# Optimization experiments

Hardware: AMD Instinct MI355X
Metric: run time of the kernel (lower is better)

The kernel has to match this reference:

```python
import jax, jax.numpy as jnp
import numpy as np

EPS = 1e-5  # torch BatchNorm1d default eps
N_NODES, N_EDGES, F_IN, HID, N_LAYERS = 100000, 1600000, 128, 128, 3


def batchnorm(x):
    # affine=False, track_running_stats=False -> normalize with batch stats (biased var)
    m = x.mean(axis=0)
    v = x.var(axis=0)
    return (x - m) / jnp.sqrt(v + EPS)


def gcn_conv(x, W, b, src, dst, deg_inv_sqrt, n):
    # PyG GCNConv: add self-loops, symmetric norm D^-1/2 (A+I) D^-1/2, then linear.
    h = x @ W  # [N, H]
    norm = deg_inv_sqrt[src] * deg_inv_sqrt[dst]  # [E]
    agg = jax.ops.segment_sum(h[src] * norm[:, None], dst, num_segments=n)
    agg = agg + h * (deg_inv_sqrt ** 2)[:, None]  # self-loop term (norm = 1/deg_i)
    return agg + b


def setup_inputs() -> dict:
    key = jax.random.key(0)
    ks = jax.random.split(key, 12)
    x = jax.random.normal(ks[0], (N_NODES, F_IN), dtype=jnp.float32)
    edge_index = jax.random.randint(ks[1], (2, N_EDGES), 0, N_NODES, dtype=jnp.int32)
    s = 1.0 / np.sqrt(F_IN)
    W0 = jax.random.uniform(ks[2], (F_IN, HID), jnp.float32, -s, s)
    b0 = jax.random.uniform(ks[3], (HID,), jnp.float32, -s, s)
    sh = 1.0 / np.sqrt(HID)
    Ws = jax.random.uniform(ks[4], (N_LAYERS - 1, HID, HID), jnp.float32, -sh, sh)
    bs = jax.random.uniform(ks[5], (N_LAYERS - 1, HID), jnp.float32, -sh, sh)
    lin1_w = jax.random.uniform(ks[6], (HID, HID), jnp.float32, -sh, sh)
    lin1_b = jax.random.uniform(ks[7], (HID,), jnp.float32, -sh, sh)
    lin2_w = jax.random.uniform(ks[8], (HID, 2), jnp.float32, -sh, sh)
    lin2_b = jax.random.uniform(ks[9], (2,), jnp.float32, -sh, sh)
    return {"x": x, "edge_index": edge_index, "W0": W0, "b0": b0, "Ws": Ws,
            "bs": bs, "lin1_w": lin1_w, "lin1_b": lin1_b, "lin2_w": lin2_w, "lin2_b": lin2_b}


def reference(x, edge_index, W0, b0, Ws, bs, lin1_w, lin1_b, lin2_w, lin2_b):
    n = x.shape[0]
    src, dst = edge_index[0], edge_index[1]
    # degree with self-loops (computed on target nodes, as in PyG)
    deg = jax.ops.segment_sum(jnp.ones_like(dst, dtype=x.dtype), dst, num_segments=n) + 1.0
    deg_inv_sqrt = deg ** -0.5
    x = jax.nn.relu(batchnorm(gcn_conv(x, W0, b0, src, dst, deg_inv_sqrt, n)))
    for i in range(Ws.shape[0]):
        x = jax.nn.relu(batchnorm(gcn_conv(x, Ws[i], bs[i], src, dst, deg_inv_sqrt, n)))
    x = jax.nn.relu(batchnorm(x @ lin1_w + lin1_b))
    return x @ lin2_w + lin2_b
```

## Files before the change

### kernel.cpp

```cpp
#include <hip/hip_runtime.h>
#include <hip/hip_fp16.h>
#include <math.h>

#define HID 128
#define EPS 1e-5f
#define NBUCK 256
#define BCAP 10240
#define TILE 8192

typedef _Float16 half8 __attribute__((ext_vector_type(8)));
typedef _Float16 half4v __attribute__((ext_vector_type(4)));
typedef float f32x4 __attribute__((ext_vector_type(4)));

__global__ __launch_bounds__(256) void setup(float* __restrict__ psums,
                                             const float* __restrict__ W0,
                                             const float* __restrict__ Ws,
                                             const float* __restrict__ lin1w,
                                             _Float16* __restrict__ Wht,
                                             int* __restrict__ bcur,
                                             _Float16* __restrict__ zrow) {
    int g = blockIdx.x * 256 + threadIdx.x;
    if (g < 4 * 65536) psums[g] = 0.f;
    if (g < 65536) {
        int m = g >> 14;
        int idx = g & 16383;
        int n = idx >> 7, k = idx & 127;
        const float* W = (m == 0) ? W0 : (m == 1) ? Ws : (m == 2) ? (Ws + 16384) : lin1w;
        Wht[(size_t)m * 16384 + n * 128 + k] = (_Float16)W[k * 128 + n];
    }
    if (g < NBUCK) bcur[g] = 0;
    if (g < 128) zrow[g] = (_Float16)0.f;
}

__global__ __launch_bounds__(512) void bin_edges(const int* __restrict__ src, const int* __restrict__ dst,
                                                 int* __restrict__ bcur, int* __restrict__ pairPack, int E) {
    __shared__ int lpack[TILE];
    __shared__ unsigned char lbuck[TILE];
    __shared__ int hist[NBUCK], hscan[NBUCK], cur[NBUCK], delta[NBUCK];
    const int t = threadIdx.x;
    const int base = blockIdx.x * TILE;

    if (t < NBUCK) hist[t] = 0;
    __syncthreads();

    int pk[16], bk[16];
#pragma unroll
    for (int i = 0; i < 16; ++i) {
        int e = base + t + 512 * i;
        if (e < E) {
            int s = src[e], d = dst[e];
            pk[i] = (s << 9) | (d & 511);
            bk[i] = d >> 9;
            atomicAdd(&hist[bk[i]], 1);
        } else {
            bk[i] = -1;
        }
    }
    __syncthreads();

    int v = (t < NBUCK) ? hist[t] : 0;
    if (t < NBUCK) hscan[t] = v;
    __syncthreads();
    for (int off = 1; off < NBUCK; off <<= 1) {
        int u = (t >= off && t < NBUCK) ? hscan[t - off] : 0;
        __syncthreads();
        if (t < NBUCK) hscan[t] += u;
        __syncthreads();
    }
    if (t < NBUCK) cur[t] = hscan[t] - v;
    __syncthreads();

#pragma unroll
    for (int i = 0; i < 16; ++i) {
        if (bk[i] >= 0) {
            int p = atomicAdd(&cur[bk[i]], 1);
            lpack[p] = pk[i];
            lbuck[p] = (unsigned char)bk[i];
        }
    }
    __syncthreads();

    if (t < NBUCK) {
        int c = hist[t];
        if (c > 0) {
            int gbase = t * BCAP + atomicAdd(&bcur[t], c);
            delta[t] = gbase - (hscan[t] - c);
        }
    }
    __syncthreads();

    int total = hscan[NBUCK - 1];
    for (int i = t; i < total; i += 512) {
        int b = lbuck[i];
        pairPack[delta[b] + i] = lpack[i];
    }
}

__global__ __launch_bounds__(512) void bucket_csr(const int* __restrict__ pairPack,
                                                  const int* __restrict__ bcur,
                                                  int* __restrict__ cnt, float* __restrict__ dis,
                                                  int* __restrict__ rowptr,
                                                  int* __restrict__ srcsort, int N) {
    __shared__ int spair[BCAP];
    __shared__ int deg[512], sc[512], cur[512];
    const int b = blockIdx.x;
    const int t = threadIdx.x;
    deg[t] = 0;
    __syncthreads();
    int n = bcur[b];
    if (n > BCAP) n = BCAP;
    const int base = b * BCAP;
    for (int i = t; i < n; i += 512) {
        int p = pairPack[base + i];
        spair[i] = p;
        atomicAdd(&deg[p & 511], 1);
    }
    __syncthreads();
    int node = b * 512 + t;
    int d = deg[t];
    sc[t] = d;
    __syncthreads();
    for (int off = 1; off < 512; off <<= 1) {
        int u = (t >= off) ? sc[t - off] : 0;
        __syncthreads();
        sc[t] += u;
        __syncthreads();
    }
    int myoff = sc[t] - d;
    cur[t] = myoff;
    if (node < N) {
        cnt[node] = d;
        dis[node] = rsqrtf((float)d + 1.0f);
        rowptr[node] = base + myoff;
    }
    __syncthreads();
    for (int i = t; i < n; i += 512) {
        int p = spair[i];
        int pos = atomicAdd(&cur[p & 511], 1);
        srcsort[base + pos] = p >> 9;
    }
}

template <bool INF16, bool NORM, bool SCALEOUT, bool STATS>
__global__ __launch_bounds__(512) void gemm_mfma(const float* __restrict__ Xf,
                                                 const _Float16* __restrict__ Xh,
                                                 const _Float16* __restrict__ Wht,
                                                 const float* __restrict__ mean, const float* __restrict__ rstd,
                                                 const float* __restrict__ dis,
                                                 _Float16* __restrict__ Yh,
                                                 float* __restrict__ psum, float* __restrict__ psumsq,
                                                 int N) {
    __shared__ _Float16 sX[128 * 136];
    __shared__ _Float16 sW[128 * 136];
    __shared__ float gsum[STATS ? 8 : 1][128], gsq[STATS ? 8 : 1][128];
    const int tid = threadIdx.x;
    const int r0 = blockIdx.x * 128;

#pragma unroll
    for (int i = 0; i < 4; ++i) {
        int f = tid + 512 * i;
        int n = f >> 4;
        int k8 = (f & 15) * 8;
        *(half8*)&sW[n * 136 + k8] = *(const half8*)&Wht[n * 128 + k8];
    }

    if (INF16) {
#pragma unroll
        for (int i = 0; i < 4; ++i) {
            int f = tid + 512 * i;
            int rr = f >> 4;
            int c8 = (f & 15) * 8;
            int gr = r0 + rr;
            half8 hv = (half8)(_Float16)0.f;
            if (gr < N) hv = *(const half8*)&Xh[(size_t)gr * 128 + c8];
            if (NORM) {
#pragma unroll
                for (int e = 0; e < 8; ++e) {
                    float u = ((float)hv[e] - mean[c8 + e]) * rstd[c8 + e];
                    hv[e] = (_Float16)fmaxf(u, 0.f);
                }
            }
            *(half8*)&sX[rr * 136 + c8] = hv;
        }
    } else {
#pragma unroll
        for (int i = 0; i < 8; ++i) {
            int f = tid + 512 * i;
            int rr = f >> 5;
            int c4 = (f & 31) * 4;
            int gr = r0 + rr;
            float4 v = make_float4(0.f, 0.f, 0.f, 0.f);
            if (gr < N) v = *(const float4*)&Xf[(size_t)gr * 128 + c4];
            if (NORM) {
                float4 m4 = *(const float4*)&mean[c4];
                float4 s4 = *(const float4*)&rstd[c4];
                v.x = fmaxf((v.x - m4.x) * s4.x, 0.f);
                v.y = fmaxf((v.y - m4.y) * s4.y, 0.f);
                v.z = fmaxf((v.z - m4.z) * s4.z, 0.f);
                v.w = fmaxf((v.w - m4.w) * s4.w, 0.f);
            }
            half4v h;
            h.x = (_Float16)v.x; h.y = (_Float16)v.y; h.z = (_Float16)v.z; h.w = (_Float16)v.w;
            *(half4v*)&sX[rr * 136 + c4] = h;
        }
    }
    __syncthreads();

    const int wv = tid >> 6;
    const int lane = tid & 63;
    const int ln = lane & 15;
    const int quad = lane >> 4;

    half8 a[4];
    {
        const _Float16* sA = &sX[(wv * 16 + ln) * 136 + quad * 8];
#pragma unroll
        for (int kc = 0; kc < 4; ++kc) a[kc] = *(const half8*)&sA[kc * 32];
    }

    f32x4 acc[8];
#pragma unroll
    for (int ct = 0; ct < 8; ++ct) acc[ct] = (f32x4){0.f, 0.f, 0.f, 0.f};

    const _Float16* wbase = &sW[ln * 136 + quad * 8];
#pragma unroll
    for (int kc = 0; kc < 4; ++kc) {
#pragma unroll
        for (int ct = 0; ct < 8; ++ct) {
            half8 b = *(const half8*)&wbase[ct * 16 * 136 + kc * 32];
            acc[ct] = __builtin_amdgcn_mfma_f32_16x16x32_f16(a[kc], b, acc[ct], 0, 0, 0);
        }
    }

    float dv[4];
    int rr[4];
#pragma unroll
    for (int rg = 0; rg < 4; ++rg) {
        rr[rg] = r0 + wv * 16 + quad * 4 + rg;
        dv[rg] = (SCALEOUT && rr[rg] < N) ? dis[rr[rg]] : 1.f;
    }

    __syncthreads();
#pragma unroll
    for (int ct = 0; ct < 8; ++ct) {
        int col = ct * 16 + ln;
#pragma unroll
        for (int rg = 0; rg < 4; ++rg)
            sX[(wv * 16 + quad * 4 + rg) * 136 + col] = (_Float16)(acc[ct][rg] * dv[rg]);
    }
    __syncthreads();
#pragma unroll
    for (int i = 0; i < 4; ++i) {
        int f = tid + 512 * i;
        int rrr = f >> 4;
        int c8 = (f & 15) * 8;
        int gr = r0 + rrr;
        if (gr < N) *(half8*)&Yh[(size_t)gr * 128 + c8] = *(const half8*)&sX[rrr * 136 + c8];
    }

    if (STATS) {
#pragma unroll
        for (int ct = 0; ct < 8; ++ct) {
            float s = 0.f, s2 = 0.f;
#pragma unroll
            for (int rg = 0; rg < 4; ++rg) {
                if (rr[rg] < N) {
                    float v = acc[ct][rg];
                    s += v;
                    s2 += v * v;
                }
            }
            s += __shfl_xor(s, 16, 64);
            s += __shfl_xor(s, 32, 64);
            s2 += __shfl_xor(s2, 16, 64);
            s2 += __shfl_xor(s2, 32, 64);
            if (quad == 0) {
                gsum[wv][ct * 16 + ln] = s;
                gsq[wv][ct * 16 + ln] = s2;
            }
        }
        __syncthreads();
        int bkt = (blockIdx.x & 7) * 128;
        if (tid < 128) {
            float s = 0.f;
#pragma unroll
            for (int i = 0; i < 8; ++i) s += gsum[i][tid];
            atomicAdd(&psum[bkt + tid], s);
        } else if (tid < 256) {
            int c = tid - 128;
            float s2 = 0.f;
#pragma unroll
            for (int i = 0; i < 8; ++i) s2 += gsq[i][c];
            atomicAdd(&psumsq[bkt + c], s2);
        }
    }
}

__global__ __launch_bounds__(256) void aggregate_f16(const __half* __restrict__ hs,
                                                     const float* __restrict__ dis,
                                                     const int* __restrict__ rowptr,
                                                     const int* __restrict__ cnt,
                                                     const int* __restrict__ srcsort,
                                                     __half* __restrict__ outP,
                                                     float* __restrict__ psum, float* __restrict__ psumsq,
                                                     int N) {
    __shared__ float asum[4][128], asq[4][128];
    const int wv = threadIdx.x >> 6;
    const int lane = threadIdx.x & 63;
    const __half2* h2 = (const __half2*)hs;
    __half2* out2 = (__half2*)outP;
    const __half2 z = __float2half2_rn(0.f);

    float sx = 0.f, sy = 0.f, qx = 0.f, qy = 0.f;

#pragma unroll
    for (int rep = 0; rep < 4; ++rep) {
        const int node = __builtin_amdgcn_readfirstlane(blockIdx.x * 16 + wv * 4 + rep);

        __half2 acch[4];
        acch[0] = h2[(size_t)node * 64 + lane];
        acch[1] = z; acch[2] = z; acch[3] = z;

        const int beg = rowptr[node];
        const int end = beg + cnt[node];
        int e = beg;
        for (; e + 16 <= end; e += 16) {
            int s[16];
#pragma unroll
            for (int j = 0; j < 16; ++j) s[j] = srcsort[e + j];
            __half2 v[16];
#pragma unroll
            for (int j = 0; j < 16; ++j) v[j] = h2[(size_t)s[j] * 64 + lane];
#pragma unroll
            for (int j = 0; j < 16; ++j) acch[j & 3] = __hadd2(acch[j & 3], v[j]);
        }
        for (; e + 4 <= end; e += 4) {
            int s[4];
#pragma unroll
            for (int j = 0; j < 4; ++j) s[j] = srcsort[e + j];
            __half2 v[4];
#pragma unroll
            for (int j = 0; j < 4; ++j) v[j] = h2[(size_t)s[j] * 64 + lane];
#pragma unroll
            for (int j = 0; j < 4; ++j) acch[j & 3] = __hadd2(acch[j & 3], v[j]);
        }
        for (; e < end; ++e) {
            acch[0] = __hadd2(acch[0], h2[(size_t)srcsort[e] * 64 + lane]);
        }

        float2 f0 = __half22float2(acch[0]);
        float2 f1 = __half22float2(acch[1]);
        float2 f2 = __half22float2(acch[2]);
        float2 f3 = __half22float2(acch[3]);
        float di = dis[node];
        float rx = ((f0.x + f1.x) + (f2.x + f3.x)) * di;
        float ry = ((f0.y + f1.y) + (f2.y + f3.y)) * di;
        out2[(size_t)node * 64 + lane] = __floats2half2_rn(rx, ry);
        sx += rx; sy += ry;
        qx += rx * rx; qy += ry * ry;
    }

    asum[wv][2 * lane] = sx;
    asum[wv][2 * lane + 1] = sy;
    asq[wv][2 * lane] = qx;
    asq[wv][2 * lane + 1] = qy;
    __syncthreads();
    const int t = threadIdx.x;
    int bkt = (blockIdx.x & 255) * 128;
    if (t < 128) {
        float s = asum[0][t] + asum[1][t] + asum[2][t] + asum[3][t];
        atomicAdd(&psum[bkt + t], s);
    } else {
        int c = t - 128;
        float s2 = asq[0][c] + asq[1][c] + asq[2][c] + asq[3][c];
        atomicAdd(&psumsq[bkt + c], s2);
    }
}

__global__ __launch_bounds__(256) void finalize_stats_par(const float* __restrict__ psum,
                                                          const float* __restrict__ psumsq,
                                                          float* __restrict__ meanf, float* __restrict__ rstdf,
                                                          int N) {
    __shared__ float ls[256], ls2[256];
    int c = blockIdx.x;
    int t = threadIdx.x;
    ls[t] = psum[t * 128 + c];
    ls2[t] = psumsq[t * 128 + c];
    __syncthreads();
    for (int off = 128; off >= 1; off >>= 1) {
        if (t < off) { ls[t] += ls[t + off]; ls2[t] += ls2[t + off]; }
        __syncthreads();
    }
    if (t == 0) {
        float m = ls[0] / (float)N;
        float var = ls2[0] / (float)N - m * m;
        meanf[c] = m;
        rstdf[c] = rsqrtf(var + EPS);
    }
}

__global__ __launch_bounds__(256) void lin2_kernel(const __half* __restrict__ Q,
                                                   const float* __restrict__ psum,
                                                   const float* __restrict__ psumsq,
                                                   const float* __restrict__ W2,
                                                   const float* __restrict__ b2, float* __restrict__ out, int N) {
    __shared__ float sw0[128], sw1[128], sm[128], srs[128];
    int t = threadIdx.x;
    if (t < 128) {
        float s = 0.f, s2 = 0.f;
#pragma unroll
        for (int b = 0; b < 8; ++b) {
            s += psum[b * 128 + t];
            s2 += psumsq[b * 128 + t];
        }
        float m = s / (float)N;
        sm[t] = m;
        srs[t] = rsqrtf(s2 / (float)N - m * m + EPS);
        sw0[t] = W2[2 * t];
        sw1[t] = W2[2 * t + 1];
    }
    __syncthreads();
    int r = blockIdx.x * 256 + t;
    if (r >= N) return;
    const __half2* q2 = (const __half2*)Q;
    float acc0 = b2[0], acc1 = b2[1];
#pragma unroll 8
    for (int k2 = 0; k2 < 64; ++k2) {
        float2 f = __half22float2(q2[(size_t)r * 64 + k2]);
        int k = 2 * k2;
        float v0 = fmaxf((f.x - sm[k]) * srs[k], 0.f);
        float v1 = fmaxf((f.y - sm[k + 1]) * srs[k + 1], 0.f);
        acc0 += v0 * sw0[k] + v1 * sw0[k + 1];
        acc1 += v0 * sw1[k] + v1 * sw1[k + 1];
    }
    *(float2*)&out[2 * r] = make_float2(acc0, acc1);
}

extern "C" void kernel_launch(void* const* d_in, const int* in_sizes, int n_in,
                              void* d_out, int out_size, void* d_ws, size_t ws_size,
                              hipStream_t stream) {
    const float* x = (const float*)d_in[0];
    const int* ei = (const int*)d_in[1];
    const float* W0 = (const float*)d_in[2];
    const float* Ws = (const float*)d_in[4];
    const float* lin1w = (const float*)d_in[6];
    const float* lin2w = (const float*)d_in[8];
    const float* lin2b = (const float*)d_in[9];
    float* out = (float*)d_out;

    const int N = in_sizes[0] / HID;
    const int E = in_sizes[1] / 2;
    const int* src = ei;
    const int* dst = ei + E;

    char* w = (char*)d_ws;
    _Float16* Hs = (_Float16*)w;     w += ((size_t)N + 1) * HID * 2;
    _Float16* P16 = (_Float16*)w;    w += (size_t)N * HID * 2;
    float* dis = (float*)w;          w += (size_t)N * 4;
    int* cnt = (int*)w;              w += (size_t)N * 4;
    int* rowptr = (int*)w;           w += (size_t)N * 4;
    int* srcsort = (int*)w;          w += (size_t)NBUCK * BCAP * 4;
    float* psums = (float*)w;        w += 4 * 65536 * 4;
    float* meanf = (float*)w;        w += 128 * 4;
    float* rstdf = (float*)w;        w += 128 * 4;
    int* bcur = (int*)w;             w += NBUCK * 4;
    _Float16* Wht = (_Float16*)w;    w += 4 * 16384 * 2;

    int* pairPack = (int*)P16;

    const __half* HsH = (const __half*)Hs;
    __half* P16H = (__half*)P16;

    const int gGemm = (N + 127) / 128;
    const int gAgg = N / 16;
    const int nBuckUsed = (N + 511) / 512;
    const int gBin = (E + TILE - 1) / TILE;

    float* ps0 = psums;
    float* ps1 = psums + 65536;
    float* ps2 = psums + 2 * 65536;
    float* ps3 = psums + 3 * 65536;

    setup<<<1024, 256, 0, stream>>>(psums, W0, Ws, lin1w, Wht, bcur, Hs + (size_t)N * HID);
    bin_edges<<<gBin, 512, 0, stream>>>(src, dst, bcur, pairPack, E);
    bucket_csr<<<nBuckUsed, 512, 0, stream>>>(pairPack, bcur, cnt, dis, rowptr, srcsort, N);

    gemm_mfma<false, false, true, false><<<gGemm, 512, 0, stream>>>(
        x, nullptr, Wht, nullptr, nullptr, dis, Hs, nullptr, nullptr, N);
    aggregate_f16<<<gAgg, 256, 0, stream>>>(HsH, dis, rowptr, cnt, srcsort, P16H, ps0, ps0 + 32768, N);
    finalize_stats_par<<<128, 256, 0, stream>>>(ps0, ps0 + 32768, meanf, rstdf, N);

    for (int l = 0; l < 2; ++l) {
        const _Float16* Wl = Wht + (size_t)(1 + l) * 16384;
        float* psl = (l == 0) ? ps1 : ps2;
        gemm_mfma<true, true, true, false><<<gGemm, 512, 0, stream>>>(
            nullptr, P16, Wl, meanf, rstdf, dis, Hs, nullptr, nullptr, N);
        aggregate_f16<<<gAgg, 256, 0, stream>>>(HsH, dis, rowptr, cnt, srcsort, P16H, psl, psl + 32768, N);
        finalize_stats_par<<<128, 256, 0, stream>>>(psl, psl + 32768, meanf, rstdf, N);
    }

    gemm_mfma<true, true, false, true><<<gGemm, 512, 0, stream>>>(
        nullptr, P16, Wht + 3 * 16384, meanf, rstdf, nullptr, Hs, ps3, ps3 + 32768, N);

    lin2_kernel<<<(N + 255) / 256, 256, 0, stream>>>(HsH, ps3, ps3 + 32768, lin2w, lin2b, out, N);
}
```

Before: 406.0 us.

## Split each node's edge list across four wave slots with 16-byte gathers

The aggregation kernel now splits each 64-lane wave into four 16-lane slots. Each slot processes a different group of 8 edges and loads a full 256-byte fp16 row as half8 vectors, where the old code had each lane load one half2 per edge. Partial sums are combined across slots with xor shuffles, and only slot 0 writes the output and accumulates the batch-norm statistics. This is meant to raise memory-level parallelism and cut per-edge instruction count for the sparse gather. Out-of-range edges are redirected to row N, which relies on that row being zero-filled, and the shuffle reduction adds some work for low-degree nodes.

Result: faster. 396.0 us (-2.4%).

```diff
diff --git a/kernel.cpp b/kernel.cpp
--- a/kernel.cpp
+++ b/kernel.cpp
@@ -296,6 +296,10 @@
     }
 }
 
+__device__ __forceinline__ int hadd2_ix(int a, int b) {
+    return __builtin_bit_cast(int, __hadd2(__builtin_bit_cast(__half2, a), __builtin_bit_cast(__half2, b)));
+}
+
 __global__ __launch_bounds__(256) void aggregate_f16(const __half* __restrict__ hs,
                                                      const float* __restrict__ dis,
                                                      const int* __restrict__ rowptr,
@@ -307,63 +311,84 @@
     __shared__ float asum[4][128], asq[4][128];
     const int wv = threadIdx.x >> 6;
     const int lane = threadIdx.x & 63;
-    const __half2* h2 = (const __half2*)hs;
-    __half2* out2 = (__half2*)outP;
-    const __half2 z = __float2half2_rn(0.f);
-
-    float sx = 0.f, sy = 0.f, qx = 0.f, qy = 0.f;
+    const int slot = lane >> 4;
+    const int chunk = lane & 15;
+    const _Float16* hsv = (const _Float16*)hs;
+    _Float16* outv = (_Float16*)outP;
+
+    float sacc[8], sqacc[8];
+#pragma unroll
+    for (int k = 0; k < 8; ++k) { sacc[k] = 0.f; sqacc[k] = 0.f; }
 
 #pragma unroll
     for (int rep = 0; rep < 4; ++rep) {
         const int node = __builtin_amdgcn_readfirstlane(blockIdx.x * 16 + wv * 4 + rep);
-
-        __half2 acch[4];
-        acch[0] = h2[(size_t)node * 64 + lane];
-        acch[1] = z; acch[2] = z; acch[3] = z;
-
         const int beg = rowptr[node];
         const int end = beg + cnt[node];
-        int e = beg;
-        for (; e + 16 <= end; e += 16) {
-            int s[16];
-#pragma unroll
-            for (int j = 0; j < 16; ++j) s[j] = srcsort[e + j];
-            __half2 v[16];
-#pragma unroll
-            for (int j = 0; j < 16; ++j) v[j] = h2[(size_t)s[j] * 64 + lane];
-#pragma unroll
-            for (int j = 0; j < 16; ++j) acch[j & 3] = __hadd2(acch[j & 3], v[j]);
-        }
-        for (; e + 4 <= end; e += 4) {
-            int s[4];
-#pragma unroll
-            for (int j = 0; j < 4; ++j) s[j] = srcsort[e + j];
-            __half2 v[4];
-#pragma unroll
-            for (int j = 0; j < 4; ++j) v[j] = h2[(size_t)s[j] * 64 + lane];
-#pragma unroll
-            for (int j = 0; j < 4; ++j) acch[j & 3] = __hadd2(acch[j & 3], v[j]);
-        }
-        for (; e < end; ++e) {
-            acch[0] = __hadd2(acch[0], h2[(size_t)srcsort[e] * 64 + lane]);
-        }
-
-        float2 f0 = __half22float2(acch[0]);
-        float2 f1 = __half22float2(acch[1]);
-        float2 f2 = __half22float2(acch[2]);
-        float2 f3 = __half22float2(acch[3]);
-        float di = dis[node];
-        float rx = ((f0.x + f1.x) + (f2.x + f3.x)) * di;
-        float ry = ((f0.y + f1.y) + (f2.y + f3.y)) * di;
-        out2[(size_t)node * 64 + lane] = __floats2half2_rn(rx, ry);
-        sx += rx; sy += ry;
-        qx += rx * rx; qy += ry * ry;
-    }
-
-    asum[wv][2 * lane] = sx;
-    asum[wv][2 * lane + 1] = sy;
-    asq[wv][2 * lane] = qx;
-    asq[wv][2 * lane + 1] = qy;
+        const float di = dis[node];
+
+        half8 acc = (half8)(_Float16)0.f;
+        if (slot == 0) acc = *(const half8*)&hsv[(size_t)node * 128 + chunk * 8];
+
+        for (int eb = beg + 8 * slot; eb < end; eb += 32) {
+            int s[8];
+#pragma unroll
+            for (int g = 0; g < 8; ++g) {
+                int e = eb + g;
+                int ce = e < end ? e : beg;
+                int sv = srcsort[ce];
+                s[g] = e < end ? sv : N;
+            }
+            half8 v[8];
+#pragma unroll
+            for (int g = 0; g < 8; ++g)
+                v[g] = *(const half8*)&hsv[(size_t)s[g] * 128 + chunk * 8];
+            half8 t0 = v[0] + v[1];
+            half8 t1 = v[2] + v[3];
+            half8 t2 = v[4] + v[5];
+            half8 t3 = v[6] + v[7];
+            acc += (t0 + t1) + (t2 + t3);
+        }
+
+        int4 u = __builtin_bit_cast(int4, acc);
+        u.x = hadd2_ix(u.x, __shfl_xor(u.x, 16, 64));
+        u.y = hadd2_ix(u.y, __shfl_xor(u.y, 16, 64));
+        u.z = hadd2_ix(u.z, __shfl_xor(u.z, 16, 64));
+        u.w = hadd2_ix(u.w, __shfl_xor(u.w, 16, 64));
+        u.x = hadd2_ix(u.x, __shfl_xor(u.x, 32, 64));
+        u.y = hadd2_ix(u.y, __shfl_xor(u.y, 32, 64));
+        u.z = hadd2_ix(u.z, __shfl_xor(u.z, 32, 64));
+        u.w = hadd2_ix(u.w, __shfl_xor(u.w, 32, 64));
+
+        float2 f0 = __half22float2(__builtin_bit_cast(__half2, u.x));
+        float2 f1 = __half22float2(__builtin_bit_cast(__half2, u.y));
+        float2 f2 = __half22float2(__builtin_bit_cast(__half2, u.z));
+        float2 f3 = __half22float2(__builtin_bit_cast(__half2, u.w));
+        float r[8];
+        r[0] = f0.x * di; r[1] = f0.y * di;
+        r[2] = f1.x * di; r[3] = f1.y * di;
+        r[4] = f2.x * di; r[5] = f2.y * di;
+        r[6] = f3.x * di; r[7] = f3.y * di;
+
+        if (slot == 0) {
+            half8 ho;
+#pragma unroll
+            for (int k = 0; k < 8; ++k) ho[k] = (_Float16)r[k];
+            *(half8*)&outv[(size_t)node * 128 + chunk * 8] = ho;
+#pragma unroll
+            for (int k = 0; k < 8; ++k) {
+                sacc[k] += r[k];
+                sqacc[k] += r[k] * r[k];
+            }
+        }
+    }
+
+    if (slot == 0) {
+        *(f32x4*)&asum[wv][chunk * 8] = (f32x4){sacc[0], sacc[1], sacc[2], sacc[3]};
+        *(f32x4*)&asum[wv][chunk * 8 + 4] = (f32x4){sacc[4], sacc[5], sacc[6], sacc[7]};
+        *(f32x4*)&asq[wv][chunk * 8] = (f32x4){sqacc[0], sqacc[1], sqacc[2], sqacc[3]};
+        *(f32x4*)&asq[wv][chunk * 8 + 4] = (f32x4){sqacc[4], sqacc[5], sqacc[6], sqacc[7]};
+    }
     __syncthreads();
     const int t = threadIdx.x;
     int bkt = (blockIdx.x & 255) * 128;
```

## Split node features into 32-column quarter planes for cache-local aggregation

Applied to the files above, without the earlier changes.

Stores intermediate fp16 node features as four column-quarter planes ([4][N][32]) instead of row-major [N][128], and updates the GEMM loads and stores and the lin2 reader to match. The aggregation kernel now assigns each block one quarter plane and gives each node 4 lanes of 16-byte loads. The goal is a smaller working set per pass, about 6.4 MB per plane, so random neighbour gathers hit in L2/MALL cache. It adds LDS atomics for the column stats, re-reads the CSR indices four times, and uses shorter per-lane gathers with less unrolling.

New measurement: 776.7 us. 1.91x slower.

```diff
diff --git a/kernel.cpp b/kernel.cpp
--- a/kernel.cpp
+++ b/kernel.cpp
@@ -7,18 +7,19 @@
 #define NBUCK 256
 #define BCAP 10240
 #define TILE 8192
+#define QSEG 32
 
 typedef _Float16 half8 __attribute__((ext_vector_type(8)));
 typedef _Float16 half4v __attribute__((ext_vector_type(4)));
 typedef float f32x4 __attribute__((ext_vector_type(4)));
+
 
 __global__ __launch_bounds__(256) void setup(float* __restrict__ psums,
                                              const float* __restrict__ W0,
                                              const float* __restrict__ Ws,
                                              const float* __restrict__ lin1w,
                                              _Float16* __restrict__ Wht,
-                                             int* __restrict__ bcur,
-                                             _Float16* __restrict__ zrow) {
+                                             int* __restrict__ bcur) {
     int g = blockIdx.x * 256 + threadIdx.x;
     if (g < 4 * 65536) psums[g] = 0.f;
     if (g < 65536) {
@@ -29,7 +30,6 @@
         Wht[(size_t)m * 16384 + n * 128 + k] = (_Float16)W[k * 128 + n];
     }
     if (g < NBUCK) bcur[g] = 0;
-    if (g < 128) zrow[g] = (_Float16)0.f;
 }
 
 __global__ __launch_bounds__(512) void bin_edges(const int* __restrict__ src, const int* __restrict__ dst,
@@ -170,9 +170,10 @@
             int f = tid + 512 * i;
             int rr = f >> 4;
             int c8 = (f & 15) * 8;
+            int q = c8 >> 5, cq = c8 & 31;
             int gr = r0 + rr;
             half8 hv = (half8)(_Float16)0.f;
-            if (gr < N) hv = *(const half8*)&Xh[(size_t)gr * 128 + c8];
+            if (gr < N) hv = *(const half8*)&Xh[(size_t)q * N * QSEG + (size_t)gr * QSEG + cq];
             if (NORM) {
 #pragma unroll
                 for (int e = 0; e < 8; ++e) {
@@ -254,8 +255,9 @@
         int f = tid + 512 * i;
         int rrr = f >> 4;
         int c8 = (f & 15) * 8;
+        int q = c8 >> 5, cq = c8 & 31;
         int gr = r0 + rrr;
-        if (gr < N) *(half8*)&Yh[(size_t)gr * 128 + c8] = *(const half8*)&sX[rrr * 136 + c8];
+        if (gr < N) *(half8*)&Yh[(size_t)q * N * QSEG + (size_t)gr * QSEG + cq] = *(const half8*)&sX[rrr * 136 + c8];
     }
 
     if (STATS) {
@@ -296,84 +298,72 @@
     }
 }
 
-__global__ __launch_bounds__(256) void aggregate_f16(const __half* __restrict__ hs,
-                                                     const float* __restrict__ dis,
-                                                     const int* __restrict__ rowptr,
-                                                     const int* __restrict__ cnt,
-                                                     const int* __restrict__ srcsort,
-                                                     __half* __restrict__ outP,
-                                                     float* __restrict__ psum, float* __restrict__ psumsq,
-                                                     int N) {
-    __shared__ float asum[4][128], asq[4][128];
+__global__ __launch_bounds__(256) void aggregate_f16q(const _Float16* __restrict__ hsq,
+                                                      const float* __restrict__ dis,
+                                                      const int* __restrict__ rowptr,
+                                                      const int* __restrict__ cnt,
+                                                      const int* __restrict__ srcsort,
+                                                      _Float16* __restrict__ outq,
+                                                      float* __restrict__ psum, float* __restrict__ psumsq,
+                                                      int N) {
+    __shared__ float colsum[32], colsq[32];
+    const int q = blockIdx.x & 3;
+    const int group = blockIdx.x >> 2;
     const int wv = threadIdx.x >> 6;
     const int lane = threadIdx.x & 63;
-    const __half2* h2 = (const __half2*)hs;
-    __half2* out2 = (__half2*)outP;
-    const __half2 z = __float2half2_rn(0.f);
-
-    float sx = 0.f, sy = 0.f, qx = 0.f, qy = 0.f;
-
-#pragma unroll
-    for (int rep = 0; rep < 4; ++rep) {
-        const int node = __builtin_amdgcn_readfirstlane(blockIdx.x * 16 + wv * 4 + rep);
-
-        __half2 acch[4];
-        acch[0] = h2[(size_t)node * 64 + lane];
-        acch[1] = z; acch[2] = z; acch[3] = z;
-
-        const int beg = rowptr[node];
-        const int end = beg + cnt[node];
-        int e = beg;
-        for (; e + 16 <= end; e += 16) {
-            int s[16];
-#pragma unroll
-            for (int j = 0; j < 16; ++j) s[j] = srcsort[e + j];
-            __half2 v[16];
-#pragma unroll
-            for (int j = 0; j < 16; ++j) v[j] = h2[(size_t)s[j] * 64 + lane];
-#pragma unroll
-            for (int j = 0; j < 16; ++j) acch[j & 3] = __hadd2(acch[j & 3], v[j]);
-        }
-        for (; e + 4 <= end; e += 4) {
-            int s[4];
-#pragma unroll
-            for (int j = 0; j < 4; ++j) s[j] = srcsort[e + j];
-            __half2 v[4];
-#pragma unroll
-            for (int j = 0; j < 4; ++j) v[j] = h2[(size_t)s[j] * 64 + lane];
-#pragma unroll
-            for (int j = 0; j < 4; ++j) acch[j & 3] = __hadd2(acch[j & 3], v[j]);
-        }
-        for (; e < end; ++e) {
-            acch[0] = __hadd2(acch[0], h2[(size_t)srcsort[e] * 64 + lane]);
-        }
-
-        float2 f0 = __half22float2(acch[0]);
-        float2 f1 = __half22float2(acch[1]);
-        float2 f2 = __half22float2(acch[2]);
-        float2 f3 = __half22float2(acch[3]);
-        float di = dis[node];
-        float rx = ((f0.x + f1.x) + (f2.x + f3.x)) * di;
-        float ry = ((f0.y + f1.y) + (f2.y + f3.y)) * di;
-        out2[(size_t)node * 64 + lane] = __floats2half2_rn(rx, ry);
-        sx += rx; sy += ry;
-        qx += rx * rx; qy += ry * ry;
-    }
-
-    asum[wv][2 * lane] = sx;
-    asum[wv][2 * lane + 1] = sy;
-    asq[wv][2 * lane] = qx;
-    asq[wv][2 * lane + 1] = qy;
-    __syncthreads();
-    const int t = threadIdx.x;
-    int bkt = (blockIdx.x & 255) * 128;
-    if (t < 128) {
-        float s = asum[0][t] + asum[1][t] + asum[2][t] + asum[3][t];
-        atomicAdd(&psum[bkt + t], s);
-    } else {
-        int c = t - 128;
-        float s2 = asq[0][c] + asq[1][c] + asq[2][c] + asq[3][c];
-        atomicAdd(&psumsq[bkt + c], s2);
+    const int slot = lane >> 2;
+    const int l4 = lane & 2 ? (lane & 3) : (lane & 3);
+    const int node = group * 64 + wv * 16 + slot;
+    const size_t pbase = (size_t)q * N * QSEG;
+
+    if (threadIdx.x < 32) { colsum[threadIdx.x] = 0.f; colsq[threadIdx.x] = 0.f; }
+    __syncthreads();
+
+    half8 acc = (half8)(_Float16)0.f;
+    float di = 0.f;
+    int beg = 0, end = 0;
+    if (node < N) {
+        beg = rowptr[node];
+        end = beg + cnt[node];
+        di = dis[node];
+        acc = *(const half8*)&hsq[pbase + (size_t)node * QSEG + l4 * 8];
+    }
+
+    int e = beg;
+    for (; e + 4 <= end; e += 4) {
+        int s0 = srcsort[e], s1 = srcsort[e + 1], s2 = srcsort[e + 2], s3 = srcsort[e + 3];
+        half8 v0 = *(const half8*)&hsq[pbase + (size_t)s0 * QSEG + l4 * 8];
+        half8 v1 = *(const half8*)&hsq[pbase + (size_t)s1 * QSEG + l4 * 8];
+        half8 v2 = *(const half8*)&hsq[pbase + (size_t)s2 * QSEG + l4 * 8];
+        half8 v3 = *(const half8*)&hsq[pbase + (size_t)s3 * QSEG + l4 * 8];
+        acc += (v0 + v1) + (v2 + v3);
+    }
+    for (; e < end; ++e) {
+        int s = srcsort[e];
+        acc += *(const half8*)&hsq[pbase + (size_t)s * QSEG + l4 * 8];
+    }
+
+    float r[8];
+#pragma unroll
+    for (int k = 0; k < 8; ++k) r[k] = (float)acc[k] * di;
+
+    if (node < N) {
+        half8 ho;
+#pragma unroll
+        for (int k = 0; k < 8; ++k) ho[k] = (_Float16)r[k];
+        *(half8*)&outq[pbase + (size_t)node * QSEG + l4 * 8] = ho;
+    }
+
+#pragma unroll
+    for (int k = 0; k < 8; ++k) {
+        atomicAdd(&colsum[l4 * 8 + k], r[k]);
+        atomicAdd(&colsq[l4 * 8 + k], r[k] * r[k]);
+    }
+    __syncthreads();
+    int bkt = (group & 255) * 128 + q * QSEG;
+    if (threadIdx.x < 32) {
+        atomicAdd(&psum[bkt + threadIdx.x], colsum[threadIdx.x]);
+        atomicAdd(&psumsq[bkt + threadIdx.x], colsq[threadIdx.x]);
     }
 }
 
@@ -424,14 +414,18 @@
     if (r >= N) return;
     const __half2* q2 = (const __half2*)Q;
     float acc0 = b2[0], acc1 = b2[1];
-#pragma unroll 8
-    for (int k2 = 0; k2 < 64; ++k2) {
-        float2 f = __half22float2(q2[(size_t)r * 64 + k2]);
-        int k = 2 * k2;
-        float v0 = fmaxf((f.x - sm[k]) * srs[k], 0.f);
-        float v1 = fmaxf((f.y - sm[k + 1]) * srs[k + 1], 0.f);
-        acc0 += v0 * sw0[k] + v1 * sw0[k + 1];
-        acc1 += v0 * sw1[k] + v1 * sw1[k + 1];
+#pragma unroll
+    for (int qp = 0; qp < 4; ++qp) {
+        size_t base2 = ((size_t)qp * N + r) * 16;
+#pragma unroll 4
+        for (int k2 = 0; k2 < 16; ++k2) {
+            float2 f = __half22float2(q2[base2 + k2]);
+            int k = qp * 32 + 2 * k2;
+            float v0 = fmaxf((f.x - sm[k]) * srs[k], 0.f);
+            float v1 = fmaxf((f.y - sm[k + 1]) * srs[k + 1], 0.f);
+            acc0 += v0 * sw0[k] + v1 * sw0[k + 1];
+            acc1 += v0 * sw1[k] + v1 * sw1[k + 1];
+        }
     }
     *(float2*)&out[2 * r] = make_float2(acc0, acc1);
 }
@@ -454,7 +448,7 @@
     const int* dst = ei + E;
 
     char* w = (char*)d_ws;
-    _Float16* Hs = (_Float16*)w;     w += ((size_t)N + 1) * HID * 2;
+    _Float16* Hs = (_Float16*)w;     w += (size_t)N * HID * 2;
     _Float16* P16 = (_Float16*)w;    w += (size_t)N * HID * 2;
     float* dis = (float*)w;          w += (size_t)N * 4;
     int* cnt = (int*)w;              w += (size_t)N * 4;
@@ -469,10 +463,10 @@
     int* pairPack = (int*)P16;
 
     const __half* HsH = (const __half*)Hs;
-    __half* P16H = (__half*)P16;
 
     const int gGemm = (N + 127) / 128;
-    const int gAgg = N / 16;
+    const int nGroups = (N + 63) / 64;
+    const int gAgg = nGroups * 4;
     const int nBuckUsed = (N + 511) / 512;
     const int gBin = (E + TILE - 1) / TILE;
 
@@ -481,13 +475,13 @@
     float* ps2 = psums + 2 * 65536;
     float* ps3 = psums + 3 * 65536;
 
-    setup<<<1024, 256, 0, stream>>>(psums, W0, Ws, lin1w, Wht, bcur, Hs + (size_t)N * HID);
+    setup<<<1024, 256, 0, stream>>>(psums, W0, Ws, lin1w, Wht, bcur);
     bin_edges<<<gBin, 512, 0, stream>>>(src, dst, bcur, pairPack, E);
     bucket_csr<<<nBuckUsed, 512, 0, stream>>>(pairPack, bcur, cnt, dis, rowptr, srcsort, N);
 
     gemm_mfma<false, false, true, false><<<gGemm, 512, 0, stream>>>(
         x, nullptr, Wht, nullptr, nullptr, dis, Hs, nullptr, nullptr, N);
-    aggregate_f16<<<gAgg, 256, 0, stream>>>(HsH, dis, rowptr, cnt, srcsort, P16H, ps0, ps0 + 32768, N);
+    aggregate_f16q<<<gAgg, 256, 0, stream>>>(Hs, dis, rowptr, cnt, srcsort, P16, ps0, ps0 + 32768, N);
     finalize_stats_par<<<128, 256, 0, stream>>>(ps0, ps0 + 32768, meanf, rstdf, N);
 
     for (int l = 0; l < 2; ++l) {
@@ -495,7 +489,7 @@
         float* psl = (l == 0) ? ps1 : ps2;
         gemm_mfma<true, true, true, false><<<gGemm, 512, 0, stream>>>(
             nullptr, P16, Wl, meanf, rstdf, dis, Hs, nullptr, nullptr, N);
-        aggregate_f16<<<gAgg, 256, 0, stream>>>(HsH, dis, rowptr, cnt, srcsort, P16H, psl, psl + 32768, N);
+        aggregate_f16q<<<gAgg, 256, 0, stream>>>(Hs, dis, rowptr, cnt, srcsort, P16, psl, psl + 32768, N);
         finalize_stats_par<<<128, 256, 0, stream>>>(psl, psl + 32768, meanf, rstdf, N);
     }
 
```
